# Performance work log

Hardware: AMD Instinct MI355X
Metric: run time of the kernel (lower is better)

## Reference

```python
import jax, jax.numpy as jnp
import numpy as np

N = 100000   # nodes
D = 128      # feature dim
E = 1600000  # edges (avg degree 16)
BN_EPS = 1e-5


def setup_inputs() -> dict:
    key = jax.random.key(0)
    ks = jax.random.split(key, 8)
    x = jax.random.normal(ks[0], (N, D), dtype=jnp.float32)
    edge_index = jax.random.randint(ks[1], (2, E), 0, N, dtype=jnp.int64)
    W = jax.random.normal(ks[2], (D, D), dtype=jnp.float32) * 0.05   # GCNConv linear weight
    b = jax.random.normal(ks[3], (D,), dtype=jnp.float32) * 0.05     # GCNConv bias
    gamma = jax.random.uniform(ks[4], (D,), dtype=jnp.float32) + 0.5 # BN weight
    beta = jax.random.normal(ks[5], (D,), dtype=jnp.float32) * 0.1   # BN bias
    running_mean = jax.random.normal(ks[6], (D,), dtype=jnp.float32) * 0.1
    running_var = jax.random.uniform(ks[7], (D,), dtype=jnp.float32) + 0.5
    return {"x": x, "edge_index": edge_index, "W": W, "b": b,
            "gamma": gamma, "beta": beta,
            "running_mean": running_mean, "running_var": running_var}


def reference(x, edge_index, W, b, gamma, beta, running_mean, running_var):
    # --- GCNConv (default: add self-loops, symmetric normalization) ---
    h = x @ W                                        # [N, D]
    loops = jnp.arange(N, dtype=edge_index.dtype)
    src = jnp.concatenate([edge_index[0], loops])    # [E+N]
    dst = jnp.concatenate([edge_index[1], loops])    # [E+N]
    deg = jax.ops.segment_sum(jnp.ones_like(dst, dtype=h.dtype), dst, num_segments=N)
    dinv = jax.lax.rsqrt(jnp.maximum(deg, 1.0))      # deg >= 1 due to self-loops
    norm = dinv[src] * dinv[dst]                     # [E+N]
    agg = jax.ops.segment_sum(h[src] * norm[:, None], dst, num_segments=N)  # [N, D]
    agg = agg + b
    # --- BatchNorm1d (inference: running stats) ---
    bn = (agg - running_mean) * jax.lax.rsqrt(running_var + BN_EPS) * gamma + beta
    # --- ReLU + residual (dropout is identity in eval) ---
    return jax.nn.relu(bn) + x
```

## Files before the change

kernel.cpp:

```cpp
#include <hip/hip_runtime.h>

#define D 128
#define BN_EPS 1e-5f
#define NBUCK 256
#define BSHIFT 9

using short8 = __attribute__((ext_vector_type(8))) short;
using floatx4 = __attribute__((ext_vector_type(4))) float;

__device__ inline unsigned short f2bf(float f) {
    unsigned u = __float_as_uint(f);
    u += 0x7fff + ((u >> 16) & 1);
    return (unsigned short)(u >> 16);
}
__device__ inline float bf2f(unsigned short s) {
    return __uint_as_float(((unsigned)s) << 16);
}

__global__ void wt_kernel(const float* __restrict__ W, const float* __restrict__ b,
                          const float* __restrict__ gamma, const float* __restrict__ beta,
                          const float* __restrict__ mean, const float* __restrict__ var,
                          unsigned short* __restrict__ Wt, float* __restrict__ scv,
                          float* __restrict__ pov, int* __restrict__ bucketTot,
                          int* __restrict__ resCnt) {
    int t = blockIdx.x * blockDim.x + threadIdx.x;
    int k = t >> 7, n = t & 127;
    Wt[(size_t)n * D + k] = f2bf(W[t]);
    if (t < D) {
        float sc = gamma[t] * rsqrtf(var[t] + BN_EPS);
        scv[t] = sc;
        pov[t] = (b[t] - mean[t]) * sc + beta[t];
    }
    if (blockIdx.x == 0 && threadIdx.x < NBUCK) {
        bucketTot[threadIdx.x] = 0;
        resCnt[threadIdx.x] = 0;
    }
}

__global__ __launch_bounds__(256) void pA_kernel(const int* __restrict__ dst,
                                                 int* __restrict__ bucketTot, int E) {
    __shared__ int lh[NBUCK];
    int tid = threadIdx.x;
    lh[tid] = 0;
    __syncthreads();
    for (int i = blockIdx.x * 256 + tid; i < E; i += gridDim.x * 256)
        atomicAdd(&lh[dst[i] >> BSHIFT], 1);
    __syncthreads();
    if (lh[tid]) atomicAdd(&bucketTot[tid], lh[tid]);
}

__global__ __launch_bounds__(256) void pB_kernel(const int* __restrict__ src,
                                                 const int* __restrict__ dst,
                                                 const int* __restrict__ bucketTot,
                                                 int* __restrict__ resCnt,
                                                 int2* __restrict__ pairs, int E) {
    __shared__ int sb[NBUCK];
    __shared__ int lh[NBUCK];
    __shared__ int lcur[NBUCK];
    int tid = threadIdx.x;
    sb[tid] = bucketTot[tid];
    lh[tid] = 0;
    __syncthreads();
    for (int d = 1; d < NBUCK; d <<= 1) {
        int v = (tid >= d) ? sb[tid - d] : 0;
        __syncthreads();
        sb[tid] += v;
        __syncthreads();
    }
    int chunk = (E + gridDim.x - 1) / gridDim.x;
    int base = blockIdx.x * chunk;
    int lim = min(chunk, E - base);
    if (lim <= 0) return;
    for (int i = tid; i < lim; i += 256) atomicAdd(&lh[dst[base + i] >> BSHIFT], 1);
    __syncthreads();
    int c = lh[tid];
    lcur[tid] = c ? (sb[tid] - bucketTot[tid]) + atomicAdd(&resCnt[tid], c) : 0;
    __syncthreads();
    for (int i = tid; i < lim; i += 256) {
        int s = src[base + i], d2 = dst[base + i];
        int pos = atomicAdd(&lcur[d2 >> BSHIFT], 1);
        pairs[pos] = make_int2(s, d2);
    }
}

__global__ __launch_bounds__(512) void sort_kernel(const int2* __restrict__ pairs,
                                                   const int* __restrict__ bucketTot,
                                                   int* __restrict__ deg,
                                                   int* __restrict__ offs,
                                                   int* __restrict__ colidx, int N, int E) {
    __shared__ int sb[NBUCK];
    __shared__ int lh[512];
    __shared__ int lcur[512];
    int tid = threadIdx.x;
    int b = blockIdx.x;
    if (tid < NBUCK) sb[tid] = bucketTot[tid];
    __syncthreads();
    for (int d = 1; d < NBUCK; d <<= 1) {
        int v = 0;
        if (tid < NBUCK && tid >= d) v = sb[tid - d];
        __syncthreads();
        if (tid < NBUCK) sb[tid] += v;
        __syncthreads();
    }
    int cnt = bucketTot[b];
    int base = sb[b] - cnt;
    lh[tid] = 0;
    __syncthreads();
    for (int i = tid; i < cnt; i += 512)
        atomicAdd(&lh[pairs[base + i].y & 511], 1);
    __syncthreads();
    int orig = lh[tid];
    for (int d = 1; d < 512; d <<= 1) {
        int v = (tid >= d) ? lh[tid - d] : 0;
        __syncthreads();
        lh[tid] += v;
        __syncthreads();
    }
    int exc = lh[tid] - orig;
    int node = b * 512 + tid;
    if (node < N) {
        deg[node] = orig;
        offs[node] = base + exc;
    }
    lcur[tid] = exc;
    if (b == 0 && tid == 0) offs[N] = E;
    __syncthreads();
    for (int i = tid; i < cnt; i += 512) {
        int2 p = pairs[base + i];
        int pos = atomicAdd(&lcur[p.y & 511], 1);
        colidx[base + pos] = p.x;
    }
}

__global__ void xs_kernel(const float* __restrict__ x, const int* __restrict__ deg,
                          float* __restrict__ dinv, unsigned short* __restrict__ xs,
                          int total4) {
    int i = blockIdx.x * blockDim.x + threadIdx.x;
    if (i >= total4) return;
    int node = i >> 5, q = i & 31;
    float dv = rsqrtf((float)(deg[node] + 1));
    if (q == 0) dinv[node] = dv;
    float4 f = ((const float4*)x)[i];
    ushort4 o;
    o.x = f2bf(dv * f.x); o.y = f2bf(dv * f.y);
    o.z = f2bf(dv * f.z); o.w = f2bf(dv * f.w);
    ((ushort4*)xs)[i] = o;
}

__global__ void deg_kernel(const int* __restrict__ dst, int* __restrict__ deg, int E) {
    int e = blockIdx.x * blockDim.x + threadIdx.x;
    if (e < E) atomicAdd(&deg[dst[e]], 1);
}

__global__ void dinv_kernel(const int* __restrict__ deg, float* __restrict__ dinv, int N) {
    int v = blockIdx.x * blockDim.x + threadIdx.x;
    if (v < N) dinv[v] = rsqrtf((float)(deg[v] + 1));
}

__global__ __launch_bounds__(256) void scan1_kernel(const int* __restrict__ deg,
                                                    int* __restrict__ bsum, int N) {
    __shared__ int s[256];
    int t = threadIdx.x;
    int v = blockIdx.x * 256 + t;
    s[t] = (v < N) ? deg[v] : 0;
    for (int st = 128; st > 0; st >>= 1) {
        __syncthreads();
        if (t < st) s[t] += s[t + st];
    }
    if (t == 0) bsum[blockIdx.x] = s[0];
}

__global__ __launch_bounds__(512) void scan2_kernel(int* __restrict__ bsum,
                                                    int* __restrict__ offs, int P, int N) {
    __shared__ int a[512];
    int t = threadIdx.x;
    int orig = (t < P) ? bsum[t] : 0;
    a[t] = orig;
    __syncthreads();
    for (int d = 1; d < 512; d <<= 1) {
        int tv = (t >= d) ? a[t - d] : 0;
        __syncthreads();
        a[t] += tv;
        __syncthreads();
    }
    if (t < P) bsum[t] = a[t] - orig;
    if (t == 0) offs[N] = a[511];
}

__global__ __launch_bounds__(256) void scan3_kernel(const int* __restrict__ deg,
                                                    const int* __restrict__ bsum,
                                                    int* __restrict__ offs,
                                                    int* __restrict__ cursor, int N) {
    __shared__ int a[256];
    int t = threadIdx.x;
    int v = blockIdx.x * 256 + t;
    int d = (v < N) ? deg[v] : 0;
    a[t] = d;
    __syncthreads();
    for (int st = 1; st < 256; st <<= 1) {
        int tv = (t >= st) ? a[t - st] : 0;
        __syncthreads();
        a[t] += tv;
        __syncthreads();
    }
    if (v < N) {
        int off = bsum[blockIdx.x] + a[t] - d;
        offs[v] = off;
        cursor[v] = off;
    }
}

__global__ void fill_kernel(const int* __restrict__ src, const int* __restrict__ dst,
                            int* __restrict__ cursor, int* __restrict__ colidx, int E) {
    int e = blockIdx.x * blockDim.x + threadIdx.x;
    if (e < E) {
        int d = dst[e];
        int pos = atomicAdd(&cursor[d], 1);
        colidx[pos] = src[e];
    }
}

__global__ __launch_bounds__(256) void agg_kernel(
    const float* __restrict__ x, const unsigned short* __restrict__ xs,
    const float* __restrict__ dinv, const int* __restrict__ offs,
    const int* __restrict__ colidx, float* __restrict__ outp,
    unsigned int* __restrict__ aggb, int N) {
    int wid = (blockIdx.x * blockDim.x + threadIdx.x) >> 6;
    if (wid >= N) return;
    int lane = threadIdx.x & 63;
    float dv = dinv[wid];
    float a0, a1;
    int p = offs[wid], pe = offs[wid + 1];
    if (xs) {
        const unsigned int* xs32 = (const unsigned int*)xs;
        unsigned int sv = xs32[(size_t)wid * 64 + lane];
        a0 = bf2f((unsigned short)sv);
        a1 = bf2f((unsigned short)(sv >> 16));
        for (; p + 16 <= pe; p += 16) {
            int u[16];
            unsigned int v[16];
#pragma unroll
            for (int j = 0; j < 16; ++j) u[j] = colidx[p + j];
#pragma unroll
            for (int j = 0; j < 16; ++j) v[j] = xs32[(size_t)u[j] * 64 + lane];
#pragma unroll
            for (int j = 0; j < 16; ++j) {
                a0 += bf2f((unsigned short)v[j]);
                a1 += bf2f((unsigned short)(v[j] >> 16));
            }
        }
        for (; p + 4 <= pe; p += 4) {
            int u[4];
            unsigned int v[4];
#pragma unroll
            for (int j = 0; j < 4; ++j) u[j] = colidx[p + j];
#pragma unroll
            for (int j = 0; j < 4; ++j) v[j] = xs32[(size_t)u[j] * 64 + lane];
#pragma unroll
            for (int j = 0; j < 4; ++j) {
                a0 += bf2f((unsigned short)v[j]);
                a1 += bf2f((unsigned short)(v[j] >> 16));
            }
        }
        for (; p < pe; ++p) {
            unsigned int v = xs32[(size_t)colidx[p] * 64 + lane];
            a0 += bf2f((unsigned short)v);
            a1 += bf2f((unsigned short)(v >> 16));
        }
        aggb[(size_t)wid * 64 + lane] =
            (unsigned int)f2bf(dv * a0) | ((unsigned int)f2bf(dv * a1) << 16);
    } else {
        const float2* x2 = (const float2*)x;
        float2 s = x2[(size_t)wid * 64 + lane];
        a0 = dv * s.x;
        a1 = dv * s.y;
        for (; p < pe; ++p) {
            int u = colidx[p];
            float du = dinv[u];
            float2 vv = x2[(size_t)u * 64 + lane];
            a0 += du * vv.x;
            a1 += du * vv.y;
        }
        float2 r;
        r.x = dv * a0;
        r.y = dv * a1;
        ((float2*)outp)[(size_t)wid * 64 + lane] = r;
    }
}

__global__ __launch_bounds__(256) void gemm_kernel(
    float* __restrict__ outp, const float* __restrict__ xg,
    const unsigned short* __restrict__ Wt, const unsigned short* __restrict__ aggb,
    const float* __restrict__ scv, const float* __restrict__ pov, int nTiles) {
    int wid = (blockIdx.x * blockDim.x + threadIdx.x) >> 6;
    if (wid >= nTiles) return;
    int lane = threadIdx.x & 63;
    int m = lane & 15, quad = lane >> 4;
    int row0 = wid * 16;

    short8 B[8][4];
#pragma unroll
    for (int cg = 0; cg < 8; ++cg)
#pragma unroll
        for (int ks = 0; ks < 4; ++ks)
            B[cg][ks] = *(const short8*)&Wt[(size_t)(cg * 16 + m) * D + ks * 32 + quad * 8];

    short8 A[4];
    if (aggb) {
        const unsigned short* arow = aggb + (size_t)(row0 + m) * D;
#pragma unroll
        for (int ks = 0; ks < 4; ++ks)
            A[ks] = *(const short8*)&arow[ks * 32 + quad * 8];
    } else {
        const float* arow = outp + (size_t)(row0 + m) * D;
#pragma unroll
        for (int ks = 0; ks < 4; ++ks) {
            float4 f0 = *(const float4*)(arow + ks * 32 + quad * 8);
            float4 f1 = *(const float4*)(arow + ks * 32 + quad * 8 + 4);
            short8 af;
            af[0] = (short)f2bf(f0.x); af[1] = (short)f2bf(f0.y);
            af[2] = (short)f2bf(f0.z); af[3] = (short)f2bf(f0.w);
            af[4] = (short)f2bf(f1.x); af[5] = (short)f2bf(f1.y);
            af[6] = (short)f2bf(f1.z); af[7] = (short)f2bf(f1.w);
            A[ks] = af;
        }
    }

#pragma unroll
    for (int cg = 0; cg < 8; ++cg) {
        floatx4 acc = {0.f, 0.f, 0.f, 0.f};
#pragma unroll
        for (int ks = 0; ks < 4; ++ks)
            acc = __builtin_amdgcn_mfma_f32_16x16x32_bf16(A[ks], B[cg][ks], acc, 0, 0, 0);
        int col = cg * 16 + m;
        float sc = scv[col], po = pov[col];
#pragma unroll
        for (int i = 0; i < 4; ++i) {
            int row = row0 + quad * 4 + i;
            float bn = acc[i] * sc + po;
            size_t idx = (size_t)row * D + col;
            outp[idx] = fmaxf(bn, 0.f) + xg[idx];
        }
    }
}

extern "C" void kernel_launch(void* const* d_in, const int* in_sizes, int n_in,
                              void* d_out, int out_size, void* d_ws, size_t ws_size,
                              hipStream_t stream) {
    const float* x = (const float*)d_in[0];
    const int* edge = (const int*)d_in[1];
    const float* Wm = (const float*)d_in[2];
    const float* b = (const float*)d_in[3];
    const float* gamma = (const float*)d_in[4];
    const float* beta = (const float*)d_in[5];
    const float* mean = (const float*)d_in[6];
    const float* var = (const float*)d_in[7];
    float* out = (float*)d_out;

    int N = in_sizes[0] / D;
    int E = in_sizes[1] / 2;
    const int* src = edge;
    const int* dst = edge + E;
    int P = (N + 255) / 256;

    char* w = (char*)d_ws;
    size_t cur = 0;
    auto take = [&](size_t bytes) -> void* {
        cur = (cur + 15) & ~(size_t)15;
        void* p = w + cur;
        cur += bytes;
        return p;
    };
    int* deg = (int*)take((size_t)N * 4);
    int* bucketTot = (int*)take(NBUCK * 4);
    int* resCnt = (int*)take(NBUCK * 4);
    float* dinv = (float*)take((size_t)N * 4);
    int* offs = (int*)take((size_t)(N + 1) * 4);
    int* cursor = (int*)take((size_t)N * 4);
    int* bsum = (int*)take((size_t)(P + 1) * 4);
    unsigned short* Wt = (unsigned short*)take((size_t)D * D * 2);
    float* scv = (float*)take(D * 4);
    float* pov = (float*)take(D * 4);
    int* colidx = (int*)take((size_t)E * 4);
    cur = (cur + 15) & ~(size_t)15;
    size_t fixedEnd = cur;

    size_t xsBytes = (size_t)N * D * 2;
    size_t zoneBytes = (xsBytes > (size_t)E * 8) ? xsBytes : (size_t)E * 8;
    bool fast = fixedEnd + xsBytes + zoneBytes <= ws_size;

    unsigned short* xs = nullptr;
    int2* pairs = nullptr;
    unsigned int* aggb = nullptr;
    if (fast) {
        xs = (unsigned short*)(w + fixedEnd);
        pairs = (int2*)(w + fixedEnd + xsBytes);
        aggb = (unsigned int*)(w + fixedEnd + xsBytes);
    }

    wt_kernel<<<(D * D) / 256, 256, 0, stream>>>(Wm, b, gamma, beta, mean, var, Wt, scv,
                                                 pov, bucketTot, resCnt);

    if (fast) {
        pA_kernel<<<1024, 256, 0, stream>>>(dst, bucketTot, E);
        pB_kernel<<<256, 256, 0, stream>>>(src, dst, bucketTot, resCnt, pairs, E);
        sort_kernel<<<NBUCK, 512, 0, stream>>>(pairs, bucketTot, deg, offs, colidx, N, E);
        xs_kernel<<<(N * 32 + 255) / 256, 256, 0, stream>>>(x, deg, dinv, xs, N * 32);
    } else {
        hipMemsetAsync(deg, 0, sizeof(int) * N, stream);
        deg_kernel<<<(E + 255) / 256, 256, 0, stream>>>(dst, deg, E);
        dinv_kernel<<<(N + 255) / 256, 256, 0, stream>>>(deg, dinv, N);
        scan1_kernel<<<P, 256, 0, stream>>>(deg, bsum, N);
        scan2_kernel<<<1, 512, 0, stream>>>(bsum, offs, P, N);
        scan3_kernel<<<P, 256, 0, stream>>>(deg, bsum, offs, cursor, N);
        fill_kernel<<<(E + 255) / 256, 256, 0, stream>>>(src, dst, cursor, colidx, E);
    }
    agg_kernel<<<(N * 64 + 255) / 256, 256, 0, stream>>>(x, xs, dinv, offs, colidx, out, aggb, N);
    int nTiles = (N + 15) / 16;
    gemm_kernel<<<(nTiles * 64 + 255) / 256, 256, 0, stream>>>(
        out, x, Wt, (const unsigned short*)aggb, scv, pov, nTiles);
}
```

Measured before the change: 299.7 us.

## Slice bf16 features into column panels for cache-local gather aggregation

Stores the scaled bf16 feature matrix as 8 column slices of 16 features each, so every slice of N nodes is about 3.2 MB. A new aggregation kernel gives each block a single slice and 8 lanes per node, so the random neighbour gathers stay within a working set small enough to remain cache-resident. The gemm reads A fragments from the sliced layout, and colidx loads and the output stores use nontemporal hints. The cost is that colidx and the offsets are re-read once per slice, and each gather is now 32 bytes per row instead of 256.

```diff
diff --git a/kernel.cpp b/kernel.cpp
--- a/kernel.cpp
+++ b/kernel.cpp
@@ -4,6 +4,7 @@
 #define BN_EPS 1e-5f
 #define NBUCK 256
 #define BSHIFT 9
+#define NSLICE 8
 
 using short8 = __attribute__((ext_vector_type(8))) short;
 using floatx4 = __attribute__((ext_vector_type(4))) float;
@@ -134,7 +135,7 @@
 
 __global__ void xs_kernel(const float* __restrict__ x, const int* __restrict__ deg,
                           float* __restrict__ dinv, unsigned short* __restrict__ xs,
-                          int total4) {
+                          int total4, int N) {
     int i = blockIdx.x * blockDim.x + threadIdx.x;
     if (i >= total4) return;
     int node = i >> 5, q = i & 31;
@@ -144,7 +145,7 @@
     ushort4 o;
     o.x = f2bf(dv * f.x); o.y = f2bf(dv * f.y);
     o.z = f2bf(dv * f.z); o.w = f2bf(dv * f.w);
-    ((ushort4*)xs)[i] = o;
+    ((ushort4*)xs)[((size_t)(q >> 2) * N + node) * 4 + (q & 3)] = o;
 }
 
 __global__ void deg_kernel(const int* __restrict__ dst, int* __restrict__ deg, int E) {
@@ -220,78 +221,91 @@
     }
 }
 
+__global__ __launch_bounds__(256, 8) void aggs_kernel(
+    const unsigned short* __restrict__ xs, const float* __restrict__ dinv,
+    const int* __restrict__ offs, const int* __restrict__ colidx,
+    unsigned int* __restrict__ aggb, int N) {
+    int slice = blockIdx.x & (NSLICE - 1);
+    int chunk = blockIdx.x >> 3;
+    int lane = threadIdx.x & 63;
+    int wv = threadIdx.x >> 6;
+    int g = lane >> 3, l = lane & 7;
+    int node = chunk * 32 + wv * 8 + g;
+    if (node >= N) return;
+
+    const unsigned int* xsb = (const unsigned int*)xs + (size_t)slice * N * 8;
+    float dv = dinv[node];
+    unsigned int sv = xsb[(size_t)node * 8 + l];
+    float a0 = bf2f((unsigned short)sv);
+    float a1 = bf2f((unsigned short)(sv >> 16));
+    int p = offs[node], pe = offs[node + 1];
+
+    for (; p + 8 <= pe; p += 8) {
+        int u[8];
+        unsigned int v[8];
+#pragma unroll
+        for (int j = 0; j < 8; ++j) u[j] = __builtin_nontemporal_load(colidx + p + j);
+#pragma unroll
+        for (int j = 0; j < 8; ++j) v[j] = xsb[(size_t)u[j] * 8 + l];
+#pragma unroll
+        for (int j = 0; j < 8; ++j) {
+            a0 += bf2f((unsigned short)v[j]);
+            a1 += bf2f((unsigned short)(v[j] >> 16));
+        }
+    }
+    for (; p + 4 <= pe; p += 4) {
+        int u[4];
+        unsigned int v[4];
+#pragma unroll
+        for (int j = 0; j < 4; ++j) u[j] = __builtin_nontemporal_load(colidx + p + j);
+#pragma unroll
+        for (int j = 0; j < 4; ++j) v[j] = xsb[(size_t)u[j] * 8 + l];
+#pragma unroll
+        for (int j = 0; j < 4; ++j) {
+            a0 += bf2f((unsigned short)v[j]);
+            a1 += bf2f((unsigned short)(v[j] >> 16));
+        }
+    }
+    for (; p < pe; ++p) {
+        unsigned int v = xsb[(size_t)__builtin_nontemporal_load(colidx + p) * 8 + l];
+        a0 += bf2f((unsigned short)v);
+        a1 += bf2f((unsigned short)(v >> 16));
+    }
+    unsigned int r =
+        (unsigned int)f2bf(dv * a0) | ((unsigned int)f2bf(dv * a1) << 16);
+    __builtin_nontemporal_store(r, aggb + (size_t)slice * N * 8 + (size_t)node * 8 + l);
+}
+
 __global__ __launch_bounds__(256) void agg_kernel(
-    const float* __restrict__ x, const unsigned short* __restrict__ xs,
-    const float* __restrict__ dinv, const int* __restrict__ offs,
-    const int* __restrict__ colidx, float* __restrict__ outp,
-    unsigned int* __restrict__ aggb, int N) {
+    const float* __restrict__ x, const float* __restrict__ dinv,
+    const int* __restrict__ offs, const int* __restrict__ colidx,
+    float* __restrict__ outp, int N) {
     int wid = (blockIdx.x * blockDim.x + threadIdx.x) >> 6;
     if (wid >= N) return;
     int lane = threadIdx.x & 63;
     float dv = dinv[wid];
-    float a0, a1;
     int p = offs[wid], pe = offs[wid + 1];
-    if (xs) {
-        const unsigned int* xs32 = (const unsigned int*)xs;
-        unsigned int sv = xs32[(size_t)wid * 64 + lane];
-        a0 = bf2f((unsigned short)sv);
-        a1 = bf2f((unsigned short)(sv >> 16));
-        for (; p + 16 <= pe; p += 16) {
-            int u[16];
-            unsigned int v[16];
-#pragma unroll
-            for (int j = 0; j < 16; ++j) u[j] = colidx[p + j];
-#pragma unroll
-            for (int j = 0; j < 16; ++j) v[j] = xs32[(size_t)u[j] * 64 + lane];
-#pragma unroll
-            for (int j = 0; j < 16; ++j) {
-                a0 += bf2f((unsigned short)v[j]);
-                a1 += bf2f((unsigned short)(v[j] >> 16));
-            }
-        }
-        for (; p + 4 <= pe; p += 4) {
-            int u[4];
-            unsigned int v[4];
-#pragma unroll
-            for (int j = 0; j < 4; ++j) u[j] = colidx[p + j];
-#pragma unroll
-            for (int j = 0; j < 4; ++j) v[j] = xs32[(size_t)u[j] * 64 + lane];
-#pragma unroll
-            for (int j = 0; j < 4; ++j) {
-                a0 += bf2f((unsigned short)v[j]);
-                a1 += bf2f((unsigned short)(v[j] >> 16));
-            }
-        }
-        for (; p < pe; ++p) {
-            unsigned int v = xs32[(size_t)colidx[p] * 64 + lane];
-            a0 += bf2f((unsigned short)v);
-            a1 += bf2f((unsigned short)(v >> 16));
-        }
-        aggb[(size_t)wid * 64 + lane] =
-            (unsigned int)f2bf(dv * a0) | ((unsigned int)f2bf(dv * a1) << 16);
-    } else {
-        const float2* x2 = (const float2*)x;
-        float2 s = x2[(size_t)wid * 64 + lane];
-        a0 = dv * s.x;
-        a1 = dv * s.y;
-        for (; p < pe; ++p) {
-            int u = colidx[p];
-            float du = dinv[u];
-            float2 vv = x2[(size_t)u * 64 + lane];
-            a0 += du * vv.x;
-            a1 += du * vv.y;
-        }
-        float2 r;
-        r.x = dv * a0;
-        r.y = dv * a1;
-        ((float2*)outp)[(size_t)wid * 64 + lane] = r;
-    }
+    const float2* x2 = (const float2*)x;
+    float2 s = x2[(size_t)wid * 64 + lane];
+    float a0 = dv * s.x;
+    float a1 = dv * s.y;
+    for (; p < pe; ++p) {
+        int u = colidx[p];
+        float du = dinv[u];
+        float2 vv = x2[(size_t)u * 64 + lane];
+        a0 += du * vv.x;
+        a1 += du * vv.y;
+    }
+    float2 r;
+    r.x = dv * a0;
+    r.y = dv * a1;
+    ((float2*)outp)[(size_t)wid * 64 + lane] = r;
 }
 
 __global__ __launch_bounds__(256) void gemm_kernel(
     float* __restrict__ outp, const float* __restrict__ xg,
     const unsigned short* __restrict__ Wt, const unsigned short* __restrict__ aggb,
-    const float* __restrict__ scv, const float* __restrict__ pov, int nTiles) {
+    const float* __restrict__ scv, const float* __restrict__ pov, int nTiles, int N) {
     int wid = (blockIdx.x * blockDim.x + threadIdx.x) >> 6;
     if (wid >= nTiles) return;
     int lane = threadIdx.x & 63;
@@ -307,10 +321,11 @@
 
     short8 A[4];
     if (aggb) {
-        const unsigned short* arow = aggb + (size_t)(row0 + m) * D;
-#pragma unroll
-        for (int ks = 0; ks < 4; ++ks)
-            A[ks] = *(const short8*)&arow[ks * 32 + quad * 8];
+#pragma unroll
+        for (int ks = 0; ks < 4; ++ks) {
+            int sl = 2 * ks + (quad >> 1);
+            A[ks] = *(const short8*)&aggb[((size_t)sl * N + row0 + m) * 16 + (quad & 1) * 8];
+        }
     } else {
         const float* arow = outp + (size_t)(row0 + m) * D;
 #pragma unroll
@@ -405,7 +420,9 @@
         pA_kernel<<<1024, 256, 0, stream>>>(dst, bucketTot, E);
         pB_kernel<<<256, 256, 0, stream>>>(src, dst, bucketTot, resCnt, pairs, E);
         sort_kernel<<<NBUCK, 512, 0, stream>>>(pairs, bucketTot, deg, offs, colidx, N, E);
-        xs_kernel<<<(N * 32 + 255) / 256, 256, 0, stream>>>(x, deg, dinv, xs, N * 32);
+        xs_kernel<<<(N * 32 + 255) / 256, 256, 0, stream>>>(x, deg, dinv, xs, N * 32, N);
+        int chunks = (N + 31) / 32;
+        aggs_kernel<<<chunks * NSLICE, 256, 0, stream>>>(xs, dinv, offs, colidx, aggb, N);
     } else {
         hipMemsetAsync(deg, 0, sizeof(int) * N, stream);
         deg_kernel<<<(E + 255) / 256, 256, 0, stream>>>(dst, deg, E);
@@ -414,9 +431,9 @@
         scan2_kernel<<<1, 512, 0, stream>>>(bsum, offs, P, N);
         scan3_kernel<<<P, 256, 0, stream>>>(deg, bsum, offs, cursor, N);
         fill_kernel<<<(E + 255) / 256, 256, 0, stream>>>(src, dst, cursor, colidx, E);
-    }
-    agg_kernel<<<(N * 64 + 255) / 256, 256, 0, stream>>>(x, xs, dinv, offs, colidx, out, aggb, N);
+        agg_kernel<<<(N * 64 + 255) / 256, 256, 0, stream>>>(x, dinv, offs, colidx, out, N);
+    }
     int nTiles = (N + 15) / 16;
     gemm_kernel<<<(nTiles * 64 + 255) / 256, 256, 0, stream>>>(
-        out, x, Wt, (const unsigned short*)aggb, scv, pov, nTiles);
-}
+        out, x, Wt, (const unsigned short*)aggb, scv, pov, nTiles, N);
+}
```

Result: slower. 366.3 us (+22.2%).
